# Optimization experiments

Hardware: AMD Instinct MI355X
Metric: run time of the kernel (lower is better)

Reference implementation:

```python
import jax, jax.numpy as jnp
import numpy as np

D_MODEL = 512
N_HEADS = 8
NUM_NODES = 20
EPS = 1e-5

def _layer_norm(x, g, b):
    mu = jnp.mean(x, axis=-1, keepdims=True)
    var = jnp.var(x, axis=-1, keepdims=True)
    return (x - mu) * jax.lax.rsqrt(var + EPS) * g + b

def _conv1d(x_bcn, w_oik):
    # x: [B, C, N], w: [O, I, K], padding = K//2 (same)
    k = w_oik.shape[-1]
    p = k // 2
    return jax.lax.conv_general_dilated(
        x_bcn, w_oik, window_strides=(1,), padding=[(p, p)],
        dimension_numbers=('NCH', 'OIH', 'NCH'))

def setup_inputs() -> dict:
    key = jax.random.key(0)
    ks = jax.random.split(key, 6)
    B, N, D, H = 4096, NUM_NODES, D_MODEL, N_HEADS
    x = jax.random.normal(ks[0], (B, N, D), dtype=jnp.float32)
    s = 1.0 / np.sqrt(D * 3)
    Wq = jax.random.normal(ks[1], (D, D, 3), dtype=jnp.float32) * s
    Wk = jax.random.normal(ks[2], (D, D, 3), dtype=jnp.float32) * s
    Wv = jax.random.normal(ks[3], (D, D, 3), dtype=jnp.float32) * s
    rel_table = jax.random.normal(ks[4], (2 * N - 1, H), dtype=jnp.float32) * 0.02
    Wo = jax.random.normal(ks[5], (D, D), dtype=jnp.float32) * (1.0 / np.sqrt(D))
    bo = jnp.zeros((D,), dtype=jnp.float32)
    ones = jnp.ones((D,), dtype=jnp.float32)
    zeros = jnp.zeros((D,), dtype=jnp.float32)
    return {"x": x, "Wq": Wq, "Wk": Wk, "Wv": Wv,
            "lnq_g": ones, "lnq_b": zeros, "lnk_g": ones, "lnk_b": zeros,
            "lnv_g": ones, "lnv_b": zeros,
            "rel_table": rel_table, "Wo": Wo, "bo": bo}

def reference(x, Wq, Wk, Wv, lnq_g, lnq_b, lnk_g, lnk_b, lnv_g, lnv_b, rel_table, Wo, bo):
    B, N, D = x.shape
    H = N_HEADS
    dk = D // H
    x_p = jnp.transpose(x, (0, 2, 1))  # [B, D, N]

    def proj(W, g, b):
        c = _conv1d(x_p, W)                      # [B, D, N]
        c = _layer_norm(jnp.transpose(c, (0, 2, 1)), g, b)  # [B, N, D]
        return x + c                              # residual

    q = proj(Wq, lnq_g, lnq_b)
    k = proj(Wk, lnk_g, lnk_b)
    v = proj(Wv, lnv_g, lnv_b)

    q = q.reshape(B, N, H, dk).transpose(0, 2, 1, 3)  # [B,H,N,dk]
    k = k.reshape(B, N, H, dk).transpose(0, 2, 1, 3)
    v = v.reshape(B, N, H, dk).transpose(0, 2, 1, 3)

    scale = 1.0 / np.sqrt(dk)
    scores = jnp.einsum('bhnd,bhmd->bhnm', q, k) * scale  # [B,H,N,N]

    # relative position bias: index[i,j] = i - j + N - 1
    coords = jnp.arange(N)
    rel_idx = coords[:, None] - coords[None, :] + (N - 1)   # [N,N]
    rel_bias = rel_table[rel_idx]                            # [N,N,H]
    rel_bias = jnp.transpose(rel_bias, (2, 0, 1))[None]      # [1,H,N,N]
    scores = scores + rel_bias

    attn = jax.nn.softmax(scores, axis=-1)
    out = jnp.einsum('bhnm,bhmd->bhnd', attn, v)             # [B,H,N,dk]
    out = out.transpose(0, 2, 1, 3).reshape(B, N, D)
    return out @ Wo.T + bo
```

## Files before the change

### kernel.cpp

```cpp
#include <hip/hip_runtime.h>
#include <hip/hip_bf16.h>
#include <stdint.h>
#include <string.h>

typedef __attribute__((ext_vector_type(8))) __bf16 bf16x8;
typedef __attribute__((ext_vector_type(4))) __bf16 bf16x4;
typedef __attribute__((ext_vector_type(4))) float f32x4;
typedef __attribute__((ext_vector_type(16))) float f32x16;

#define B_TOT   4096
#define NN      20
#define DM      512
#define NC1     1536
#define M_TOT   (B_TOT*NN)
#define NPAD    22

__device__ __forceinline__ void async_copy16(const __bf16* g, __bf16* l) {
    __builtin_amdgcn_global_load_lds(
        (__attribute__((address_space(1))) void*)g,
        (__attribute__((address_space(3))) void*)l, 16, 0, 0);
}

template<typename T>
__device__ __forceinline__ void load8(const T* p, float* r) {
    if constexpr (sizeof(T) == 4) {
        f32x4 a = *(const f32x4*)p;
        f32x4 b = *(const f32x4*)(p + 4);
#pragma unroll
        for (int i = 0; i < 4; ++i) { r[i] = a[i]; r[i + 4] = b[i]; }
    } else {
        bf16x8 a = *(const bf16x8*)p;
#pragma unroll
        for (int i = 0; i < 8; ++i) r[i] = (float)a[i];
    }
}

__device__ __forceinline__ bf16x8 zero8() {
    bf16x8 z;
#pragma unroll
    for (int i = 0; i < 8; ++i) z[i] = (__bf16)0.f;
    return z;
}

__device__ __forceinline__ uint32_t pkbf(float a, float b) {
    __bf16 x = (__bf16)a, y = (__bf16)b;
    uint16_t ux, uy;
    __builtin_memcpy(&ux, &x, 2); __builtin_memcpy(&uy, &y, 2);
    return (uint32_t)ux | ((uint32_t)uy << 16);
}

__device__ __forceinline__ bf16x8 mkfrag(uint32_t w0, uint32_t w1, uint32_t w2, uint32_t w3) {
    union { uint32_t u[4]; bf16x8 v; } X;
    X.u[0] = w0; X.u[1] = w1; X.u[2] = w2; X.u[3] = w3;
    return X.v;
}

__global__ void detect_kernel(const uint32_t* __restrict__ xw, int* __restrict__ mode) {
    int lane = threadIdx.x & 63;
    int susp = 0;
#pragma unroll
    for (int i = 0; i < 4; ++i) {
        uint32_t w = xw[lane * 4 + i];
        uint32_t e = (w >> 7) & 0xFF;
        if ((e >= 118 && e <= 130) || (w & 0xFFFFu) == 0) susp++;
    }
#pragma unroll
    for (int o = 32; o > 0; o >>= 1) susp += __shfl_xor(susp, o, 64);
    if (lane == 0) *mode = (susp > 128) ? 1 : 0;
}

template<typename T>
__device__ __forceinline__ void wt_body(
    const T* __restrict__ Wq, const T* __restrict__ Wk, const T* __restrict__ Wv,
    const T* __restrict__ Wo, __bf16* __restrict__ Wt, __bf16* __restrict__ Wob, int t)
{
    if (t < 3 * 512 * 512) {
        int p = t >> 18;
        int r = t & 262143;
        int o = r >> 9, i = r & 511;
        const T* W = (p == 0) ? Wq : ((p == 1) ? Wk : Wv);
        const T* src = W + (size_t)(o * 512 + i) * 3;
        float w0 = (float)src[0], w1 = (float)src[1], w2 = (float)src[2];
        size_t base = (size_t)(p * 512 + o) * 1536 + i;
        Wt[base]        = (__bf16)w0;
        Wt[base + 512]  = (__bf16)w1;
        Wt[base + 1024] = (__bf16)w2;
    } else {
        int g2 = t - 3 * 512 * 512;
        Wob[g2] = (__bf16)(float)Wo[g2];
    }
}

__global__ __launch_bounds__(256) void wt_kernel(
    const void* Wq, const void* Wk, const void* Wv, const void* Wo,
    __bf16* Wt, __bf16* Wob, const int* mode)
{
    int t = blockIdx.x * 256 + threadIdx.x;
    if (*mode)
        wt_body<__bf16>((const __bf16*)Wq, (const __bf16*)Wk, (const __bf16*)Wv,
                        (const __bf16*)Wo, Wt, Wob, t);
    else
        wt_body<float>((const float*)Wq, (const float*)Wk, (const float*)Wv,
                       (const float*)Wo, Wt, Wob, t);
}

template<typename T>
__device__ __forceinline__ void xpad_body(
    const T* __restrict__ x, __bf16* __restrict__ xp, int idx)
{
    int col = (idx & 63) * 8;
    int row = idx >> 6;
    int b = row / 22;
    int np = row - b * 22;
    bf16x8 ov;
    if (np == 0 || np == 21) {
        ov = zero8();
    } else {
        float tmp[8];
        load8<T>(x + ((size_t)(b * 20 + np - 1) * 512 + col), tmp);
#pragma unroll
        for (int t = 0; t < 8; ++t) ov[t] = (__bf16)tmp[t];
    }
    *(bf16x8*)(xp + (size_t)row * 512 + col) = ov;
}

__global__ __launch_bounds__(256) void xpad_kernel(
    const void* x, __bf16* xp, const int* mode)
{
    int idx = blockIdx.x * 256 + threadIdx.x;
    if (*mode) xpad_body<__bf16>((const __bf16*)x, xp, idx);
    else       xpad_body<float>((const float*)x, xp, idx);
}

#define SBAR()  __builtin_amdgcn_s_barrier()
#define SCHED0() __builtin_amdgcn_sched_barrier(0)
#define LGKM0() do { asm volatile("s_waitcnt lgkmcnt(0)" ::: "memory"); SCHED0(); } while (0)
#define VM4()   do { SCHED0(); asm volatile("s_waitcnt vmcnt(4)" ::: "memory"); } while (0)
#define VM0()   do { SCHED0(); asm volatile("s_waitcnt vmcnt(0)" ::: "memory"); } while (0)

__device__ __forceinline__ void g1_loadA(const __bf16* slab, int off, bf16x8 (&aq)[4]) {
#pragma unroll
    for (int i = 0; i < 4; ++i) aq[i] = *(const bf16x8*)(slab + off + i * 512);
}
__device__ __forceinline__ void g1_loadB(const __bf16* slab, int off, bf16x8 (&bq)[4]) {
#pragma unroll
    for (int i = 0; i < 4; ++i) bq[i] = *(const bf16x8*)(slab + off + i * 512);
}
template<int QM>
__device__ __forceinline__ void g1_mma(bf16x8 (&aq)[4], bf16x8 (&bq)[4], f32x4 (&acc)[8][4]) {
    __builtin_amdgcn_s_setprio(1);
#pragma unroll
    for (int i = 0; i < 4; ++i)
#pragma unroll
        for (int nf = 0; nf < 4; ++nf)
            acc[QM * 4 + i][nf] = __builtin_amdgcn_mfma_f32_16x16x32_bf16(
                aq[i], bq[nf], acc[QM * 4 + i][nf], 0, 0, 0);
    __builtin_amdgcn_s_setprio(0);
}

template<int NT>
__device__ __forceinline__ void kloop8(
    const __bf16* aP0, const __bf16* aP1, const __bf16* bP0, const __bf16* bP1,
    __bf16* shA, __bf16* shB, int sdst, int rdA, int rdB, f32x4 (&acc)[8][4])
{
    bf16x8 aq[4], bq[4];
    { __bf16* d = shA + 0 * 8192 + sdst; async_copy16(aP0 + 0, d);  async_copy16(aP1 + 0, d + 4096); }
    { __bf16* d = shB + 0 * 8192 + sdst; async_copy16(bP0 + 0, d);  async_copy16(bP1 + 0, d + 4096); }
    { __bf16* d = shA + 1 * 8192 + sdst; async_copy16(aP0 + 32, d); async_copy16(aP1 + 32, d + 4096); }
    { __bf16* d = shB + 1 * 8192 + sdst; async_copy16(bP0 + 32, d); async_copy16(bP1 + 32, d + 4096); }
    VM4();
    SBAR();

    for (int t = 0; t < NT; ++t) {
        const int cur = t & 1;
        const __bf16* A0 = shA + (cur * 2 + 0) * 8192;
        const __bf16* A1 = shA + (cur * 2 + 1) * 8192;
        const __bf16* B0 = shB + (cur * 2 + 0) * 8192;
        const __bf16* B1 = shB + (cur * 2 + 1) * 8192;
        __bf16* dA0 = shA + ((cur ^ 1) * 2 + 0) * 8192 + sdst;
        __bf16* dA1 = shA + ((cur ^ 1) * 2 + 1) * 8192 + sdst;
        __bf16* dB0 = shB + ((cur ^ 1) * 2 + 0) * 8192 + sdst;
        __bf16* dB1 = shB + ((cur ^ 1) * 2 + 1) * 8192 + sdst;
        const int kn = (t + 1) * 64;
        const bool st = (t < NT - 1);

        g1_loadA(A0, rdA, aq);
        g1_loadB(B0, rdB, bq);
        if (st) { async_copy16(aP0 + kn, dA0); async_copy16(aP1 + kn, dA0 + 4096); }
        SBAR(); LGKM0();
        g1_mma<0>(aq, bq, acc);
        SBAR();

        g1_loadA(A0, rdA + 2048, aq);
        if (st) { async_copy16(bP0 + kn, dB0); async_copy16(bP1 + kn, dB0 + 4096); }
        if (st) VM4(); else VM0();
        SBAR(); LGKM0();
        g1_mma<1>(aq, bq, acc);
        SBAR();

        g1_loadA(A1, rdA, aq);
        g1_loadB(B1, rdB, bq);
        if (st) { async_copy16(aP0 + kn + 32, dA1); async_copy16(aP1 + kn + 32, dA1 + 4096); }
        SBAR(); LGKM0();
        g1_mma<0>(aq, bq, acc);
        SBAR();

        g1_loadA(A1, rdA + 2048, aq);
        if (st) { async_copy16(bP0 + kn + 32, dB1); async_copy16(bP1 + kn + 32, dB1 + 4096); }
        if (st) VM4();
        SBAR(); LGKM0();
        g1_mma<1>(aq, bq, acc);
        SBAR();
    }
}

__global__ __launch_bounds__(512, 2) void g1_kernel(
    const __bf16* __restrict__ xpad, const __bf16* __restrict__ Wt,
    __bf16* __restrict__ Cout, int mbase)
{
    extern __shared__ __align__(16) __bf16 sh[];
    __bf16* shA = sh;
    __bf16* shB = sh + 32768;

    const int tid = threadIdx.x;
    const int w = tid >> 6, l = tid & 63;
    const int lr = l & 15, lq = l >> 4;
    const int wm = w >> 2, wn = w & 3;

    int nwg = gridDim.x;
    int bid = blockIdx.x;
    if ((nwg & 7) == 0) bid = (bid & 7) * (nwg >> 3) + (bid >> 3);
    const int nb = bid % 6;
    const int mb = bid / 6;
    const int n0 = nb * 256;
    const int mloc = mb * 256;

    const int rin = l >> 2;
    const int pc  = (l & 3) * 8;
    const int lc  = (rin >= 8) ? (pc ^ 16) : pc;
    const int R0 = w * 16 + rin;
    const int R1 = 128 + R0;
    const int g0 = mbase + mloc + R0, g1r = mbase + mloc + R1;
    const __bf16* aP0 = xpad + (size_t)((g0 / 20) * 22 + g0 % 20) * 512 + lc;
    const __bf16* aP1 = xpad + (size_t)((g1r / 20) * 22 + g1r % 20) * 512 + lc;
    const __bf16* bP0 = Wt + (size_t)(n0 + R0) * 1536 + lc;
    const __bf16* bP1 = Wt + (size_t)(n0 + R1) * 1536 + lc;
    const int sdst = w * 512 + l * 8;

    const int swzcol = (lr >= 8) ? ((lq * 8) ^ 16) : (lq * 8);
    const int ardoff = lr * 32 + swzcol;
    const int rdA = wm * 8 * 512 + ardoff;
    const int rdB = wn * 4 * 512 + ardoff;

    f32x4 acc[8][4] = {};
    kloop8<24>(aP0, aP1, bP0, bP1, shA, shB, sdst, rdA, rdB, acc);

#pragma unroll
    for (int mf = 0; mf < 8; ++mf) {
#pragma unroll
        for (int r = 0; r < 4; ++r) {
            int row = mloc + wm * 128 + mf * 16 + lq * 4 + r;
            size_t base = (size_t)row * 1536 + n0 + wn * 64 + lr;
#pragma unroll
            for (int nf = 0; nf < 4; ++nf)
                Cout[base + nf * 16] = (__bf16)acc[mf][nf][r];
        }
    }
}

template<typename T>
__device__ __forceinline__ void attn_body(
    const __bf16* __restrict__ xpad, const __bf16* __restrict__ cqkv,
    const T* __restrict__ lnq_g, const T* __restrict__ lnq_b,
    const T* __restrict__ lnk_g, const T* __restrict__ lnk_b,
    const T* __restrict__ lnv_g, const T* __restrict__ lnv_b,
    const T* __restrict__ rel, __bf16* __restrict__ aout, int bbase,
    __bf16* sq , __bf16* vT ,
    float* rbt )
{
    const int tid = threadIdx.x;
    const int wave = tid >> 6, lane = tid & 63;
    const int bl = blockIdx.x;
    char* sqb = (char*)sq;
    char* vTb = (char*)vT;
    const size_t xpbase = ((size_t)(bbase + bl) * NPAD + 1) * DM;
    const size_t cbase = (size_t)bl * NN * NC1;

#pragma unroll
    for (int k = 0; k < 4; ++k)
        *(bf16x8*)(vTb + tid * 64 + k * 16) = zero8();
    if (tid < 312) {
        int h = tid & 7, d = tid >> 3;
        rbt[h * 40 + d] = (float)rel[tid];
    }
    __syncthreads();

#pragma unroll
    for (int p = 0; p < 3; ++p) {
        const T* gp = (p == 0) ? lnq_g : (p == 1) ? lnk_g : lnv_g;
        const T* bp = (p == 0) ? lnq_b : (p == 1) ? lnk_b : lnv_b;
        float gv[8], bv[8];
        load8<T>(gp + lane * 8, gv);
        load8<T>(bp + lane * 8, bv);
        bf16x8 cvv[3], xvv[3];
#pragma unroll
        for (int rr = 0; rr < 3; ++rr) {
            int n = wave + rr * 8;
            if (n < 20) {
                cvv[rr] = *(const bf16x8*)(cqkv + cbase + (size_t)n * NC1 + p * 512 + lane * 8);
                xvv[rr] = *(const bf16x8*)(xpad + xpbase + (size_t)n * DM + lane * 8);
            }
        }
#pragma unroll
        for (int rr = 0; rr < 3; ++rr) {
            int n = wave + rr * 8;
            if (n < 20) {
                float vals[8]; float s1 = 0.f, s2 = 0.f;
#pragma unroll
                for (int t = 0; t < 8; ++t) { float f = (float)cvv[rr][t]; vals[t] = f; s1 += f; s2 += f * f; }
#pragma unroll
                for (int o = 32; o > 0; o >>= 1) { s1 += __shfl_xor(s1, o, 64); s2 += __shfl_xor(s2, o, 64); }
                float mu = s1 * (1.f / 512.f);
                float var = s2 * (1.f / 512.f) - mu * mu;
                float rs = rsqrtf(var + 1e-5f);
                bf16x8 ov;
#pragma unroll
                for (int t = 0; t < 8; ++t)
                    ov[t] = (__bf16)((vals[t] - mu) * rs * gv[t] + bv[t] + (float)xvv[rr][t]);
                if (p < 2) {
                    int row = p * 20 + n;
                    *(bf16x8*)(sqb + row * 1024 + ((lane * 16) ^ ((row & 31) << 4))) = ov;
                } else {
#pragma unroll
                    for (int t = 0; t < 8; ++t) {
                        int c = lane * 8 + t;
                        unsigned short ub;
                        __bf16 b = ov[t];
                        __builtin_memcpy(&ub, &b, 2);
                        *(unsigned short*)(vTb + c * 64 + ((n * 2) ^ (((c >> 3) & 3) << 4))) = ub;
                    }
                }
            }
        }
    }
    __syncthreads();

    const int h  = wave;
    const int ic = lane & 31;
    const int lq = lane >> 5;

    f32x16 s;
#pragma unroll
    for (int r = 0; r < 16; ++r) s[r] = 0.f;
#pragma unroll
    for (int call = 0; call < 4; ++call) {
        int kb2 = (call * 16 + lq * 8) * 2;
        bf16x8 af = zero8(), bf_ = zero8();
        if (ic < 20) {
            int rk = 20 + ic;
            af  = *(const bf16x8*)(sqb + rk * 1024 + ((h * 128 + kb2) ^ ((rk & 31) << 4)));
            bf_ = *(const bf16x8*)(sqb + ic * 1024 + ((h * 128 + kb2) ^ ((ic & 31) << 4)));
        }
        s = __builtin_amdgcn_mfma_f32_32x32x16_bf16(af, bf_, s, 0, 0, 0);
    }
    __syncthreads();

    {
        float mx = -1e30f;
#pragma unroll
        for (int r = 0; r < 16; ++r) {
            int j = (r & 3) + 8 * (r >> 2) + 4 * lq;
            if (j < 20) {
                int d = ic - j + 19;
                d = d < 0 ? 0 : (d > 38 ? 38 : d);
                s[r] = s[r] * 0.125f + rbt[h * 40 + d];
                mx = fmaxf(mx, s[r]);
            } else s[r] = -1e30f;
        }
        mx = fmaxf(mx, __shfl_xor(mx, 32, 64));
        float sum = 0.f;
#pragma unroll
        for (int r = 0; r < 16; ++r) {
            int j = (r & 3) + 8 * (r >> 2) + 4 * lq;
            float e = (j < 20) ? __expf(s[r] - mx) : 0.f;
            s[r] = e; sum += e;
        }
        sum += __shfl_xor(sum, 32, 64);
        float inv = 1.f / sum;
#pragma unroll
        for (int r = 0; r < 16; ++r) s[r] *= inv;
    }

    bf16x8 pa1, pa2;
    {
        uint32_t pk[8], qk[8];
#pragma unroll
        for (int k = 0; k < 8; ++k) pk[k] = pkbf(s[2 * k], s[2 * k + 1]);
#pragma unroll
        for (int k = 0; k < 8; ++k) qk[k] = (uint32_t)__shfl_xor((int)pk[k], 32, 64);
        pa1 = lq ? mkfrag(qk[2], qk[3], pk[2], pk[3]) : mkfrag(pk[0], pk[1], qk[0], qk[1]);
        pa2 = lq ? mkfrag(qk[6], qk[7], pk[6], pk[7]) : mkfrag(pk[4], pk[5], qk[4], qk[5]);
    }

#pragma unroll 1
    for (int ct = 0; ct < 2; ++ct) {
        const int cb0 = h * 64 + ct * 32;
        const int c_a = cb0 + ic;
        const int arow = c_a * 64;
        const int aswz = ((c_a >> 3) & 3) << 4;
        bf16x8 a1 = *(const bf16x8*)(vTb + arow + ((lq * 16 + 0)  ^ aswz));
        bf16x8 a2 = *(const bf16x8*)(vTb + arow + ((lq * 16 + 32) ^ aswz));
        f32x16 o;
#pragma unroll
        for (int r = 0; r < 16; ++r) o[r] = 0.f;
        o = __builtin_amdgcn_mfma_f32_32x32x16_bf16(a1, pa1, o, 0, 0, 0);
        o = __builtin_amdgcn_mfma_f32_32x32x16_bf16(a2, pa2, o, 0, 0, 0);
        if (ic < 20) {
#pragma unroll
            for (int g2 = 0; g2 < 4; ++g2) {
                int c0 = cb0 + 8 * g2 + 4 * lq;
                bf16x4 ov4;
#pragma unroll
                for (int e = 0; e < 4; ++e) ov4[e] = (__bf16)o[g2 * 4 + e];
                *(bf16x4*)(sqb + ic * 1024 + ((c0 * 2) ^ ((ic & 31) << 4))) = ov4;
            }
        }
    }
    __syncthreads();

    __bf16* ab = aout + (size_t)bl * NN * DM;
    for (int t = tid; t < 1280; t += 512) {
        int row = t >> 6;
        int bc = (t & 63) * 16;
        bf16x8 vv = *(const bf16x8*)(sqb + row * 1024 + (bc ^ ((row & 31) << 4)));
        *(bf16x8*)(ab + t * 8) = vv;
    }
}

__global__ __launch_bounds__(512, 4) void attn_kernel(
    const __bf16* xpad, const __bf16* cqkv,
    const void* lnq_g, const void* lnq_b, const void* lnk_g, const void* lnk_b,
    const void* lnv_g, const void* lnv_b, const void* rel,
    __bf16* aout, int bbase, const int* mode)
{
    __shared__ __align__(16) __bf16 sq[40 * 512];
    __shared__ __align__(16) __bf16 vT[512 * 32];
    __shared__ float rbt[8 * 40];
    if (*mode)
        attn_body<__bf16>(xpad, cqkv,
            (const __bf16*)lnq_g, (const __bf16*)lnq_b, (const __bf16*)lnk_g,
            (const __bf16*)lnk_b, (const __bf16*)lnv_g, (const __bf16*)lnv_b,
            (const __bf16*)rel, aout, bbase, sq, vT, rbt);
    else
        attn_body<float>(xpad, cqkv,
            (const float*)lnq_g, (const float*)lnq_b, (const float*)lnk_g,
            (const float*)lnk_b, (const float*)lnv_g, (const float*)lnv_b,
            (const float*)rel, aout, bbase, sq, vT, rbt);
}

template<typename T>
__device__ __forceinline__ void g3_body(
    const __bf16* __restrict__ Ain, const __bf16* __restrict__ Wob,
    const T* __restrict__ bo, T* __restrict__ out, int mbase, __bf16* sh)
{
    __bf16* shA = sh;
    __bf16* shB = sh + 32768;

    const int tid = threadIdx.x;
    const int w = tid >> 6, l = tid & 63;
    const int lr = l & 15, lq = l >> 4;
    const int wm = w >> 2, wn = w & 3;

    int nwg = gridDim.x;
    int bid = blockIdx.x;
    if ((nwg & 7) == 0) bid = (bid & 7) * (nwg >> 3) + (bid >> 3);
    const int nb = bid & 1;
    const int mb = bid >> 1;
    const int n0 = nb * 256;
    const int mloc = mb * 256;

    const int rin = l >> 2;
    const int pc  = (l & 3) * 8;
    const int lc  = (rin >= 8) ? (pc ^ 16) : pc;
    const int R0 = w * 16 + rin;
    const int R1 = 128 + R0;
    const __bf16* aP0 = Ain + (size_t)(mloc + R0) * 512 + lc;
    const __bf16* aP1 = Ain + (size_t)(mloc + R1) * 512 + lc;
    const __bf16* bP0 = Wob + (size_t)(n0 + R0) * 512 + lc;
    const __bf16* bP1 = Wob + (size_t)(n0 + R1) * 512 + lc;
    const int sdst = w * 512 + l * 8;

    const int swzcol = (lr >= 8) ? ((lq * 8) ^ 16) : (lq * 8);
    const int ardoff = lr * 32 + swzcol;
    const int rdA = wm * 8 * 512 + ardoff;
    const int rdB = wn * 4 * 512 + ardoff;

    f32x4 acc[8][4] = {};
    kloop8<8>(aP0, aP1, bP0, bP1, shA, shB, sdst, rdA, rdB, acc);

    float bias[4];
#pragma unroll
    for (int nf = 0; nf < 4; ++nf) bias[nf] = (float)bo[n0 + wn * 64 + lr + nf * 16];
#pragma unroll
    for (int mf = 0; mf < 8; ++mf) {
#pragma unroll
        for (int r = 0; r < 4; ++r) {
            int row = mloc + wm * 128 + mf * 16 + lq * 4 + r;
            size_t gbase = (size_t)(mbase + row) * 512 + n0 + wn * 64 + lr;
#pragma unroll
            for (int nf = 0; nf < 4; ++nf)
                out[gbase + nf * 16] = (T)(acc[mf][nf][r] + bias[nf]);
        }
    }
}

__global__ __launch_bounds__(512, 2) void g3_kernel(
    const __bf16* Ain, const __bf16* Wob, const void* bo, void* out,
    int mbase, const int* mode)
{
    extern __shared__ __align__(16) __bf16 sh3[];
    if (*mode) g3_body<__bf16>(Ain, Wob, (const __bf16*)bo, (__bf16*)out, mbase, sh3);
    else       g3_body<float>(Ain, Wob, (const float*)bo, (float*)out, mbase, sh3);
}

extern "C" void kernel_launch(void* const* d_in, const int* in_sizes, int n_in,
                              void* d_out, int out_size, void* d_ws, size_t ws_size,
                              hipStream_t stream) {
    (void)in_sizes; (void)n_in; (void)out_size; (void)ws_size;
    char* ws = (char*)d_ws;
    int*    mode = (int*)ws;
    __bf16* Wt   = (__bf16*)(ws + 256);
    __bf16* Wob  = (__bf16*)(ws + 256 + 4718592);
    __bf16* xpad = (__bf16*)(ws + 256 + 4718592 + 524288);
    const size_t off_c = 256 + 4718592 + 524288 + (size_t)B_TOT * NPAD * DM * 2;

    static bool attr_set = false;
    if (!attr_set) {
        (void)hipFuncSetAttribute((const void*)g1_kernel,
                                  hipFuncAttributeMaxDynamicSharedMemorySize, 131072);
        (void)hipFuncSetAttribute((const void*)g3_kernel,
                                  hipFuncAttributeMaxDynamicSharedMemorySize, 131072);
        attr_set = true;
    }

    __bf16* Cbuf = (__bf16*)(ws + off_c);
    __bf16* Abuf = (__bf16*)(ws + off_c + (size_t)M_TOT * NC1 * 2);

    detect_kernel<<<dim3(1), dim3(64), 0, stream>>>((const uint32_t*)d_in[0], mode);
    wt_kernel<<<dim3(4096), dim3(256), 0, stream>>>(
        d_in[1], d_in[2], d_in[3], d_in[11], Wt, Wob, mode);
    xpad_kernel<<<dim3(22528), dim3(256), 0, stream>>>(d_in[0], xpad, mode);

    g1_kernel<<<dim3(6 * (M_TOT / 256)), dim3(512), 131072, stream>>>(
        xpad, Wt, Cbuf, 0);
    attn_kernel<<<dim3(B_TOT), dim3(512), 0, stream>>>(
        xpad, Cbuf, d_in[4], d_in[5], d_in[6], d_in[7], d_in[8], d_in[9],
        d_in[10], Abuf, 0, mode);
    g3_kernel<<<dim3(2 * (M_TOT / 256)), dim3(512), 131072, stream>>>(
        Abuf, Wob, d_in[12], d_out, 0, mode);
}
```

Before: 823.9 us.

## Make attention kernel persistent with register prefetch of next batch item

The attention kernel now launches 512 blocks, and each block loops over 8 batch items instead of one block per item. Inside the loop it prefetches the next item's conv outputs and residual rows into registers while the current item's attention runs. This amortises the per-block setup (zeroing vT, the rel-bias table) and hides global-load latency behind compute. In exchange it holds 12 bf16x8 vectors in registers, which may cut occupancy under launch_bounds(512,4), and it adds an extra barrier per iteration.

```diff
diff --git a/kernel.cpp b/kernel.cpp
--- a/kernel.cpp
+++ b/kernel.cpp
@@ -14,6 +14,8 @@
 #define NC1     1536
 #define M_TOT   (B_TOT*NN)
 #define NPAD    22
+#define AGRID   512
+#define AITER   (B_TOT/AGRID)
 
 __device__ __forceinline__ void async_copy16(const __bf16* g, __bf16* l) {
     __builtin_amdgcn_global_load_lds(
@@ -278,13 +280,12 @@
     __bf16* sq , __bf16* vT ,
     float* rbt )
 {
+    (void)bbase;
     const int tid = threadIdx.x;
     const int wave = tid >> 6, lane = tid & 63;
     const int bl = blockIdx.x;
     char* sqb = (char*)sq;
     char* vTb = (char*)vT;
-    const size_t xpbase = ((size_t)(bbase + bl) * NPAD + 1) * DM;
-    const size_t cbase = (size_t)bl * NN * NC1;
 
 #pragma unroll
     for (int k = 0; k < 4; ++k)
@@ -293,147 +294,185 @@
         int h = tid & 7, d = tid >> 3;
         rbt[h * 40 + d] = (float)rel[tid];
     }
-    __syncthreads();
-
-#pragma unroll
-    for (int p = 0; p < 3; ++p) {
-        const T* gp = (p == 0) ? lnq_g : (p == 1) ? lnk_g : lnv_g;
-        const T* bp = (p == 0) ? lnq_b : (p == 1) ? lnk_b : lnv_b;
-        float gv[8], bv[8];
-        load8<T>(gp + lane * 8, gv);
-        load8<T>(bp + lane * 8, bv);
-        bf16x8 cvv[3], xvv[3];
+
+    const int h  = wave;
+    const int ic = lane & 31;
+    const int lq = lane >> 5;
+
+    bf16x8 cvv[9], xvv[3];
+
+    {
+        const size_t cb0 = (size_t)bl * NN * NC1;
+        const size_t xb0 = ((size_t)bl * NPAD + 1) * DM;
+#pragma unroll
+        for (int p = 0; p < 3; ++p)
+#pragma unroll
+            for (int rr = 0; rr < 3; ++rr) {
+                int n = wave + rr * 8;
+                if (n < 20)
+                    cvv[p * 3 + rr] = *(const bf16x8*)(cqkv + cb0 + (size_t)n * NC1 + p * 512 + lane * 8);
+            }
 #pragma unroll
         for (int rr = 0; rr < 3; ++rr) {
             int n = wave + rr * 8;
-            if (n < 20) {
-                cvv[rr] = *(const bf16x8*)(cqkv + cbase + (size_t)n * NC1 + p * 512 + lane * 8);
-                xvv[rr] = *(const bf16x8*)(xpad + xpbase + (size_t)n * DM + lane * 8);
-            }
-        }
-#pragma unroll
-        for (int rr = 0; rr < 3; ++rr) {
-            int n = wave + rr * 8;
-            if (n < 20) {
-                float vals[8]; float s1 = 0.f, s2 = 0.f;
-#pragma unroll
-                for (int t = 0; t < 8; ++t) { float f = (float)cvv[rr][t]; vals[t] = f; s1 += f; s2 += f * f; }
-#pragma unroll
-                for (int o = 32; o > 0; o >>= 1) { s1 += __shfl_xor(s1, o, 64); s2 += __shfl_xor(s2, o, 64); }
-                float mu = s1 * (1.f / 512.f);
-                float var = s2 * (1.f / 512.f) - mu * mu;
-                float rs = rsqrtf(var + 1e-5f);
-                bf16x8 ov;
-#pragma unroll
-                for (int t = 0; t < 8; ++t)
-                    ov[t] = (__bf16)((vals[t] - mu) * rs * gv[t] + bv[t] + (float)xvv[rr][t]);
-                if (p < 2) {
-                    int row = p * 20 + n;
-                    *(bf16x8*)(sqb + row * 1024 + ((lane * 16) ^ ((row & 31) << 4))) = ov;
-                } else {
-#pragma unroll
-                    for (int t = 0; t < 8; ++t) {
-                        int c = lane * 8 + t;
-                        unsigned short ub;
-                        __bf16 b = ov[t];
-                        __builtin_memcpy(&ub, &b, 2);
-                        *(unsigned short*)(vTb + c * 64 + ((n * 2) ^ (((c >> 3) & 3) << 4))) = ub;
+            if (n < 20)
+                xvv[rr] = *(const bf16x8*)(xpad + xb0 + (size_t)n * DM + lane * 8);
+        }
+    }
+    __syncthreads();
+
+#pragma unroll 1
+    for (int it = 0; it < AITER; ++it) {
+        const int item = it * AGRID + bl;
+
+#pragma unroll
+        for (int p = 0; p < 3; ++p) {
+            const T* gp = (p == 0) ? lnq_g : (p == 1) ? lnk_g : lnv_g;
+            const T* bp = (p == 0) ? lnq_b : (p == 1) ? lnk_b : lnv_b;
+            float gv[8], bv[8];
+            load8<T>(gp + lane * 8, gv);
+            load8<T>(bp + lane * 8, bv);
+#pragma unroll
+            for (int rr = 0; rr < 3; ++rr) {
+                int n = wave + rr * 8;
+                if (n < 20) {
+                    float vals[8]; float s1 = 0.f, s2 = 0.f;
+#pragma unroll
+                    for (int t = 0; t < 8; ++t) { float f = (float)cvv[p * 3 + rr][t]; vals[t] = f; s1 += f; s2 += f * f; }
+#pragma unroll
+                    for (int o = 32; o > 0; o >>= 1) { s1 += __shfl_xor(s1, o, 64); s2 += __shfl_xor(s2, o, 64); }
+                    float mu = s1 * (1.f / 512.f);
+                    float var = s2 * (1.f / 512.f) - mu * mu;
+                    float rs = rsqrtf(var + 1e-5f);
+                    bf16x8 ov;
+#pragma unroll
+                    for (int t = 0; t < 8; ++t)
+                        ov[t] = (__bf16)((vals[t] - mu) * rs * gv[t] + bv[t] + (float)xvv[rr][t]);
+                    if (p < 2) {
+                        int row = p * 20 + n;
+                        *(bf16x8*)(sqb + row * 1024 + ((lane * 16) ^ ((row & 31) << 4))) = ov;
+                    } else {
+#pragma unroll
+                        for (int t = 0; t < 8; ++t) {
+                            int c = lane * 8 + t;
+                            unsigned short ub;
+                            __bf16 b = ov[t];
+                            __builtin_memcpy(&ub, &b, 2);
+                            *(unsigned short*)(vTb + c * 64 + ((n * 2) ^ (((c >> 3) & 3) << 4))) = ub;
+                        }
                     }
                 }
             }
         }
-    }
-    __syncthreads();
-
-    const int h  = wave;
-    const int ic = lane & 31;
-    const int lq = lane >> 5;
-
-    f32x16 s;
-#pragma unroll
-    for (int r = 0; r < 16; ++r) s[r] = 0.f;
-#pragma unroll
-    for (int call = 0; call < 4; ++call) {
-        int kb2 = (call * 16 + lq * 8) * 2;
-        bf16x8 af = zero8(), bf_ = zero8();
-        if (ic < 20) {
-            int rk = 20 + ic;
-            af  = *(const bf16x8*)(sqb + rk * 1024 + ((h * 128 + kb2) ^ ((rk & 31) << 4)));
-            bf_ = *(const bf16x8*)(sqb + ic * 1024 + ((h * 128 + kb2) ^ ((ic & 31) << 4)));
-        }
-        s = __builtin_amdgcn_mfma_f32_32x32x16_bf16(af, bf_, s, 0, 0, 0);
-    }
-    __syncthreads();
-
-    {
-        float mx = -1e30f;
-#pragma unroll
-        for (int r = 0; r < 16; ++r) {
-            int j = (r & 3) + 8 * (r >> 2) + 4 * lq;
-            if (j < 20) {
-                int d = ic - j + 19;
-                d = d < 0 ? 0 : (d > 38 ? 38 : d);
-                s[r] = s[r] * 0.125f + rbt[h * 40 + d];
-                mx = fmaxf(mx, s[r]);
-            } else s[r] = -1e30f;
-        }
-        mx = fmaxf(mx, __shfl_xor(mx, 32, 64));
-        float sum = 0.f;
-#pragma unroll
-        for (int r = 0; r < 16; ++r) {
-            int j = (r & 3) + 8 * (r >> 2) + 4 * lq;
-            float e = (j < 20) ? __expf(s[r] - mx) : 0.f;
-            s[r] = e; sum += e;
-        }
-        sum += __shfl_xor(sum, 32, 64);
-        float inv = 1.f / sum;
-#pragma unroll
-        for (int r = 0; r < 16; ++r) s[r] *= inv;
-    }
-
-    bf16x8 pa1, pa2;
-    {
-        uint32_t pk[8], qk[8];
-#pragma unroll
-        for (int k = 0; k < 8; ++k) pk[k] = pkbf(s[2 * k], s[2 * k + 1]);
-#pragma unroll
-        for (int k = 0; k < 8; ++k) qk[k] = (uint32_t)__shfl_xor((int)pk[k], 32, 64);
-        pa1 = lq ? mkfrag(qk[2], qk[3], pk[2], pk[3]) : mkfrag(pk[0], pk[1], qk[0], qk[1]);
-        pa2 = lq ? mkfrag(qk[6], qk[7], pk[6], pk[7]) : mkfrag(pk[4], pk[5], qk[4], qk[5]);
-    }
+
+        if (it + 1 < AITER) {
+            const int nitem = (it + 1) * AGRID + bl;
+            const size_t cbn = (size_t)nitem * NN * NC1;
+            const size_t xbn = ((size_t)nitem * NPAD + 1) * DM;
+#pragma unroll
+            for (int p = 0; p < 3; ++p)
+#pragma unroll
+                for (int rr = 0; rr < 3; ++rr) {
+                    int n = wave + rr * 8;
+                    if (n < 20)
+                        cvv[p * 3 + rr] = *(const bf16x8*)(cqkv + cbn + (size_t)n * NC1 + p * 512 + lane * 8);
+                }
+#pragma unroll
+            for (int rr = 0; rr < 3; ++rr) {
+                int n = wave + rr * 8;
+                if (n < 20)
+                    xvv[rr] = *(const bf16x8*)(xpad + xbn + (size_t)n * DM + lane * 8);
+            }
+        }
+        __syncthreads();
+
+        f32x16 s;
+#pragma unroll
+        for (int r = 0; r < 16; ++r) s[r] = 0.f;
+#pragma unroll
+        for (int call = 0; call < 4; ++call) {
+            int kb2 = (call * 16 + lq * 8) * 2;
+            bf16x8 af = zero8(), bf_ = zero8();
+            if (ic < 20) {
+                int rk = 20 + ic;
+                af  = *(const bf16x8*)(sqb + rk * 1024 + ((h * 128 + kb2) ^ ((rk & 31) << 4)));
+                bf_ = *(const bf16x8*)(sqb + ic * 1024 + ((h * 128 + kb2) ^ ((ic & 31) << 4)));
+            }
+            s = __builtin_amdgcn_mfma_f32_32x32x16_bf16(af, bf_, s, 0, 0, 0);
+        }
+        __syncthreads();
+
+        {
+            float mx = -1e30f;
+#pragma unroll
+            for (int r = 0; r < 16; ++r) {
+                int j = (r & 3) + 8 * (r >> 2) + 4 * lq;
+                if (j < 20) {
+                    int d = ic - j + 19;
+                    d = d < 0 ? 0 : (d > 38 ? 38 : d);
+                    s[r] = s[r] * 0.125f + rbt[h * 40 + d];
+                    mx = fmaxf(mx, s[r]);
+                } else s[r] = -1e30f;
+            }
+            mx = fmaxf(mx, __shfl_xor(mx, 32, 64));
+            float sum = 0.f;
+#pragma unroll
+            for (int r = 0; r < 16; ++r) {
+                int j = (r & 3) + 8 * (r >> 2) + 4 * lq;
+                float e = (j < 20) ? __expf(s[r] - mx) : 0.f;
+                s[r] = e; sum += e;
+            }
+            sum += __shfl_xor(sum, 32, 64);
+            float inv = 1.f / sum;
+#pragma unroll
+            for (int r = 0; r < 16; ++r) s[r] *= inv;
+        }
+
+        bf16x8 pa1, pa2;
+        {
+            uint32_t pk[8], qk[8];
+#pragma unroll
+            for (int k = 0; k < 8; ++k) pk[k] = pkbf(s[2 * k], s[2 * k + 1]);
+#pragma unroll
+            for (int k = 0; k < 8; ++k) qk[k] = (uint32_t)__shfl_xor((int)pk[k], 32, 64);
+            pa1 = lq ? mkfrag(qk[2], qk[3], pk[2], pk[3]) : mkfrag(pk[0], pk[1], qk[0], qk[1]);
+            pa2 = lq ? mkfrag(qk[6], qk[7], pk[6], pk[7]) : mkfrag(pk[4], pk[5], qk[4], qk[5]);
+        }
 
 #pragma unroll 1
-    for (int ct = 0; ct < 2; ++ct) {
-        const int cb0 = h * 64 + ct * 32;
-        const int c_a = cb0 + ic;
-        const int arow = c_a * 64;
-        const int aswz = ((c_a >> 3) & 3) << 4;
-        bf16x8 a1 = *(const bf16x8*)(vTb + arow + ((lq * 16 + 0)  ^ aswz));
-        bf16x8 a2 = *(const bf16x8*)(vTb + arow + ((lq * 16 + 32) ^ aswz));
-        f32x16 o;
-#pragma unroll
-        for (int r = 0; r < 16; ++r) o[r] = 0.f;
-        o = __builtin_amdgcn_mfma_f32_32x32x16_bf16(a1, pa1, o, 0, 0, 0);
-        o = __builtin_amdgcn_mfma_f32_32x32x16_bf16(a2, pa2, o, 0, 0, 0);
-        if (ic < 20) {
-#pragma unroll
-            for (int g2 = 0; g2 < 4; ++g2) {
-                int c0 = cb0 + 8 * g2 + 4 * lq;
-                bf16x4 ov4;
-#pragma unroll
-                for (int e = 0; e < 4; ++e) ov4[e] = (__bf16)o[g2 * 4 + e];
-                *(bf16x4*)(sqb + ic * 1024 + ((c0 * 2) ^ ((ic & 31) << 4))) = ov4;
+        for (int ct = 0; ct < 2; ++ct) {
+            const int cb0 = h * 64 + ct * 32;
+            const int c_a = cb0 + ic;
+            const int arow = c_a * 64;
+            const int aswz = ((c_a >> 3) & 3) << 4;
+            bf16x8 a1 = *(const bf16x8*)(vTb + arow + ((lq * 16 + 0)  ^ aswz));
+            bf16x8 a2 = *(const bf16x8*)(vTb + arow + ((lq * 16 + 32) ^ aswz));
+            f32x16 o;
+#pragma unroll
+            for (int r = 0; r < 16; ++r) o[r] = 0.f;
+            o = __builtin_amdgcn_mfma_f32_32x32x16_bf16(a1, pa1, o, 0, 0, 0);
+            o = __builtin_amdgcn_mfma_f32_32x32x16_bf16(a2, pa2, o, 0, 0, 0);
+            if (ic < 20) {
+#pragma unroll
+                for (int g2 = 0; g2 < 4; ++g2) {
+                    int c0 = cb0 + 8 * g2 + 4 * lq;
+                    bf16x4 ov4;
+#pragma unroll
+                    for (int e = 0; e < 4; ++e) ov4[e] = (__bf16)o[g2 * 4 + e];
+                    *(bf16x4*)(sqb + ic * 1024 + ((c0 * 2) ^ ((ic & 31) << 4))) = ov4;
+                }
             }
         }
-    }
-    __syncthreads();
-
-    __bf16* ab = aout + (size_t)bl * NN * DM;
-    for (int t = tid; t < 1280; t += 512) {
-        int row = t >> 6;
-        int bc = (t & 63) * 16;
-        bf16x8 vv = *(const bf16x8*)(sqb + row * 1024 + (bc ^ ((row & 31) << 4)));
-        *(bf16x8*)(ab + t * 8) = vv;
+        __syncthreads();
+
+        __bf16* ab = aout + (size_t)item * NN * DM;
+        for (int t = tid; t < 1280; t += 512) {
+            int row = t >> 6;
+            int bc = (t & 63) * 16;
+            bf16x8 vv = *(const bf16x8*)(sqb + row * 1024 + (bc ^ ((row & 31) << 4)));
+            *(bf16x8*)(ab + t * 8) = vv;
+        }
+        __syncthreads();
     }
 }
 
@@ -553,7 +592,7 @@
 
     g1_kernel<<<dim3(6 * (M_TOT / 256)), dim3(512), 131072, stream>>>(
         xpad, Wt, Cbuf, 0);
-    attn_kernel<<<dim3(B_TOT), dim3(512), 0, stream>>>(
+    attn_kernel<<<dim3(AGRID), dim3(512), 0, stream>>>(
         xpad, Cbuf, d_in[4], d_in[5], d_in[6], d_in[7], d_in[8], d_in[9],
         d_in[10], Abuf, 0, mode);
     g3_kernel<<<dim3(2 * (M_TOT / 256)), dim3(512), 131072, stream>>>(
```

Result: slower. 980.1 us (+19.0%).
